# Performance work log

Hardware: AMD Instinct MI355X
Metric: run time of the kernel (lower is better)

## Reference

```python
import jax, jax.numpy as jnp
import numpy as np

NH = 16          # num_attention_heads
NOPE = 128       # qk_nope_head_dim
ROPE = 64        # qk_rope_head_dim
QHD = NOPE + ROPE  # q_head_dim = 192
VD = 128         # v_head_dim
QLR = 1536       # q_lora_rank
KVLR = 512       # kv_lora_rank
HID = 2048
B, S = 1, 2048
THETA = 10000.0
EPS = 1e-6


def rms_norm(x, w, eps=EPS):
    xf = x.astype(jnp.float32)
    var = jnp.mean(xf * xf, axis=-1, keepdims=True)
    return (w * (xf * jax.lax.rsqrt(var + eps)).astype(x.dtype))


def _deinterleave(x):
    # view(..., d//2, 2).transpose(-1, -2).reshape(..., d): evens then odds
    return jnp.concatenate([x[..., 0::2], x[..., 1::2]], axis=-1)


def _rotate_half(x):
    h = x.shape[-1] // 2
    return jnp.concatenate([-x[..., h:], x[..., :h]], axis=-1)


def setup_inputs() -> dict:
    key = jax.random.key(0)
    ks = jax.random.split(key, 6)
    s = 0.02
    return {
        'hidden_states': jax.random.normal(ks[0], (B, S, HID), jnp.float32),
        'position_ids': jnp.arange(S, dtype=jnp.int32)[None, :],
        'Wqa': jax.random.normal(ks[1], (HID, QLR), jnp.float32) * s,
        'qa_ln_w': jnp.ones((QLR,), jnp.float32),
        'Wqb': jax.random.normal(ks[2], (QLR, NH * QHD), jnp.float32) * s,
        'Wkva': jax.random.normal(ks[3], (HID, KVLR + ROPE), jnp.float32) * s,
        'kv_ln_w': jnp.ones((KVLR,), jnp.float32),
        'Wkvb': jax.random.normal(ks[4], (KVLR, NH * (NOPE + VD)), jnp.float32) * s,
        'Wo': jax.random.normal(ks[5], (NH * VD, HID), jnp.float32) * s,
    }


def reference(hidden_states, position_ids, Wqa, qa_ln_w, Wqb, Wkva, kv_ln_w, Wkvb, Wo):
    b, s, _ = hidden_states.shape
    # Q path: low-rank down -> RMSNorm -> up
    q = rms_norm(hidden_states @ Wqa, qa_ln_w) @ Wqb
    q = q.reshape(b, s, NH, QHD).transpose(0, 2, 1, 3)          # (b,h,s,192)
    q_nope, q_pe = q[..., :NOPE], q[..., NOPE:]
    # KV path: compressed kv + shared rope key
    ckv = hidden_states @ Wkva                                   # (b,s,576)
    c_kv, k_pe = ckv[..., :KVLR], ckv[..., KVLR:]
    k_pe = k_pe.reshape(b, s, 1, ROPE).transpose(0, 2, 1, 3)     # (b,1,s,64)
    kv = rms_norm(c_kv, kv_ln_w) @ Wkvb
    kv = kv.reshape(b, s, NH, NOPE + VD).transpose(0, 2, 1, 3)   # (b,h,s,256)
    k_nope, v = kv[..., :NOPE], kv[..., NOPE:]
    # partial RoPE on the 64-dim rope slices
    inv_freq = 1.0 / (THETA ** (jnp.arange(0, ROPE, 2, dtype=jnp.float32) / ROPE))
    t = jnp.arange(s, dtype=jnp.float32)
    emb = jnp.concatenate([jnp.outer(t, inv_freq)] * 2, axis=-1)  # (s,64)
    cos = jnp.cos(emb)[position_ids][:, None]                     # (b,1,s,64)
    sin = jnp.sin(emb)[position_ids][:, None]
    q_pe = _deinterleave(q_pe)
    k_pe = _deinterleave(k_pe)
    q_pe = q_pe * cos + _rotate_half(q_pe) * sin
    k_pe = k_pe * cos + _rotate_half(k_pe) * sin
    query = jnp.concatenate([q_nope, q_pe], axis=-1)                       # (b,h,s,192)
    key = jnp.concatenate([k_nope, jnp.broadcast_to(k_pe, (b, NH, s, ROPE))], axis=-1)
    # causal attention, softmax_scale = q_head_dim**-0.5
    scale = QHD ** (-0.5)
    scores = jnp.einsum('bhqd,bhkd->bhqk', query, key) * scale
    mask = jnp.tril(jnp.ones((s, s), dtype=bool))
    scores = jnp.where(mask, scores, jnp.finfo(scores.dtype).min)
    probs = jax.nn.softmax(scores, axis=-1)
    attn = jnp.einsum('bhqk,bhkd->bhqd', probs, v)               # (b,h,s,128)
    out = attn.transpose(0, 2, 1, 3).reshape(b, s, NH * VD) @ Wo  # (b,s,hid)
    return out
```

## Files before the change

### kernel.cpp

```cpp
#include <hip/hip_runtime.h>
#include <hip/hip_bf16.h>

typedef unsigned short u16;
typedef _Float16 h16;
typedef h16 h16x8 __attribute__((ext_vector_type(8)));
typedef h16 h16x4 __attribute__((ext_vector_type(4)));
typedef float f32x4 __attribute__((ext_vector_type(4)));

#define S_LEN 2048
#define QLR   1536
#define KVLR  512
#define NHEAD 16
#define QHD   192
#define QHS   200
#define VDIM  128
#define SCALE 0.07216878364870322f
#define FREQC (-0.4152410118609203f)

__device__ __forceinline__ void gld16(const h16* g, h16* l){
  __builtin_amdgcn_global_load_lds((__attribute__((address_space(1))) const void*)g,
                                   (__attribute__((address_space(3))) void*)l, 16, 0, 0);
}

__global__ __launch_bounds__(256) void k_cvt(const float* __restrict__ in, h16* __restrict__ out, int n4){
  int i = blockIdx.x * 256 + threadIdx.x;
  if (i < n4){
    float4 v = ((const float4*)in)[i];
    h16x4 o = { (h16)v.x, (h16)v.y, (h16)v.z, (h16)v.w };
    ((h16x4*)out)[i] = o;
  }
}

__global__ __launch_bounds__(256) void k_tc(const float* __restrict__ W, h16* __restrict__ WT, int K, int N){
  __shared__ float t[64][65];
  int k0 = blockIdx.y * 64, n0 = blockIdx.x * 64;
  int tid = threadIdx.x;
  int r = tid >> 4, c4 = (tid & 15) * 4;
#pragma unroll
  for (int it = 0; it < 4; it++){
    float4 v = *(const float4*)(W + (size_t)(k0 + it*16 + r) * N + n0 + c4);
    t[it*16+r][c4] = v.x; t[it*16+r][c4+1] = v.y; t[it*16+r][c4+2] = v.z; t[it*16+r][c4+3] = v.w;
  }
  __syncthreads();
  int n = tid >> 2, k16 = (tid & 3) * 16;
  h16x8 o0, o1;
#pragma unroll
  for (int e = 0; e < 8; e++){ o0[e] = (h16)t[k16 + e][n]; o1[e] = (h16)t[k16 + 8 + e][n]; }
  h16* dst = WT + (size_t)(n0 + n) * K + k0 + k16;
  *(h16x8*)dst = o0;
  *(h16x8*)(dst + 8) = o1;
}

__device__ __forceinline__ void gemm_core(const h16* __restrict__ A, const h16* __restrict__ B,
    int K, int m0, int n0, h16* As, h16* Bs, f32x4 (&acc)[4][4]){
  const int tid = threadIdx.x;
  const int lane = tid & 63, quad = lane >> 4, lr = lane & 15;
  const int wid = tid >> 6;
  const int wr = (wid >> 1) * 64, wc = (wid & 1) * 64;
  const int sr = tid >> 2, scc = (tid & 3) * 8;
  const h16* Ag = A + (size_t)(m0 + sr) * K + scc;
  const h16* Bg = B + (size_t)(n0 + sr) * K + scc;
  for (int kt = 0; kt < K; kt += 32){
    gld16(Ag + kt,                 &As[tid * 8]);
    gld16(Ag + (size_t)64*K + kt,  &As[2048 + tid * 8]);
    gld16(Bg + kt,                 &Bs[tid * 8]);
    gld16(Bg + (size_t)64*K + kt,  &Bs[2048 + tid * 8]);
    __syncthreads();
    h16x8 af[4], bfr[4];
#pragma unroll
    for (int r = 0; r < 4; r++) af[r]  = *(const h16x8*)&As[(wr + r*16 + lr) * 32 + quad * 8];
#pragma unroll
    for (int c = 0; c < 4; c++) bfr[c] = *(const h16x8*)&Bs[(wc + c*16 + lr) * 32 + quad * 8];
#pragma unroll
    for (int r = 0; r < 4; r++)
#pragma unroll
      for (int c = 0; c < 4; c++)
        acc[r][c] = __builtin_amdgcn_mfma_f32_16x16x32_f16(af[r], bfr[c], acc[r][c], 0, 0, 0);
    __syncthreads();
  }
}

template<bool OF32>
__global__ __launch_bounds__(256) void k_gemm(const h16* __restrict__ A, const h16* __restrict__ B,
                                              void* __restrict__ Cv, int N, int K){
  __shared__ __attribute__((aligned(16))) h16 As[128*32];
  __shared__ __attribute__((aligned(16))) h16 Bs[128*32];
  const int m0 = blockIdx.y * 128, n0 = blockIdx.x * 128;
  f32x4 acc[4][4] = {};
  gemm_core(A, B, K, m0, n0, As, Bs, acc);
  const int lane = threadIdx.x & 63, quad = lane >> 4, lr = lane & 15;
  const int wid = threadIdx.x >> 6;
  const int wr = (wid >> 1) * 64, wc = (wid & 1) * 64;
#pragma unroll
  for (int r = 0; r < 4; r++)
#pragma unroll
    for (int c = 0; c < 4; c++){
      int row = m0 + wr + r*16 + quad*4;
      int col = n0 + wc + c*16 + lr;
#pragma unroll
      for (int i = 0; i < 4; i++){
        float val = acc[r][c][i];
        if (OF32) ((float*)Cv)[(size_t)(row + i) * N + col] = val;
        else      ((h16*)Cv)[(size_t)(row + i) * N + col] = (h16)val;
      }
    }
}

__global__ __launch_bounds__(256) void k_gemm_q(const h16* __restrict__ A, const h16* __restrict__ B,
      h16* __restrict__ Qh, const float* __restrict__ cst, const float* __restrict__ snt){
  __shared__ __attribute__((aligned(16))) h16 As[128*32];
  __shared__ __attribute__((aligned(16))) h16 Bs[128*32];
  const int m0 = blockIdx.y * 128, n0 = blockIdx.x * 128;
  f32x4 acc[4][4] = {};
  gemm_core(A, B, QLR, m0, n0, As, Bs, acc);
  const int lane = threadIdx.x & 63, quad = lane >> 4, lr = lane & 15;
  const int wid = threadIdx.x >> 6;
  const int wr = (wid >> 1) * 64, wc = (wid & 1) * 64;
#pragma unroll
  for (int r = 0; r < 4; r++)
#pragma unroll
    for (int c = 0; c < 4; c++){
      int row0 = m0 + wr + r*16 + quad*4;
      int cg = n0 + wc + c*16 + lr;
      int head = cg / 192;
      int inner = cg - head*192;
      h16* outb = Qh + ((size_t)head*S_LEN)*QHS;
      if (inner < 128){
#pragma unroll
        for (int i = 0; i < 4; i++)
          outb[(size_t)(row0+i)*QHS + inner] = (h16)(acc[r][c][i] * SCALE);
      } else {
        int d = (inner - 128) >> 1;
        int isY = inner & 1;
        int ocol = (isY ? 160 : 128) + d;
#pragma unroll
        for (int i = 0; i < 4; i++){
          int rr = row0 + i;
          float cs = cst[rr*32 + d], sn = snt[rr*32 + d];
          float v = acc[r][c][i];
          float w = __shfl_xor(v, 1);
          float out = isY ? (v*cs + w*sn) : (v*cs - w*sn);
          outb[(size_t)rr*QHS + ocol] = (h16)(out * SCALE);
        }
      }
    }
}

__global__ __launch_bounds__(256) void k_gemm_kv(const h16* __restrict__ A, const h16* __restrict__ B,
      h16* __restrict__ Kh, h16* __restrict__ VT){
  __shared__ __attribute__((aligned(16))) h16 As[128*32];
  __shared__ __attribute__((aligned(16))) h16 Bs[128*32];
  __shared__ __attribute__((aligned(16))) h16 tsm[128*132];
  const int m0 = blockIdx.y * 128, n0 = blockIdx.x * 128;
  f32x4 acc[4][4] = {};
  gemm_core(A, B, KVLR, m0, n0, As, Bs, acc);
  const int tid = threadIdx.x;
  const int lane = tid & 63, quad = lane >> 4, lr = lane & 15;
  const int wid = tid >> 6;
  const int wr = (wid >> 1) * 64, wc = (wid & 1) * 64;
  const int head = n0 >> 8;
  if ((n0 & 128) == 0){
#pragma unroll
    for (int r = 0; r < 4; r++)
#pragma unroll
      for (int c = 0; c < 4; c++){
        int row0 = m0 + wr + r*16 + quad*4;
        int inner = wc + c*16 + lr;
#pragma unroll
        for (int i = 0; i < 4; i++)
          Kh[((size_t)head*S_LEN + row0 + i)*QHS + inner] = (h16)acc[r][c][i];
      }
  } else {
#pragma unroll
    for (int r = 0; r < 4; r++)
#pragma unroll
      for (int c = 0; c < 4; c++){
        int lrow = wr + r*16 + quad*4;
        int dv = wc + c*16 + lr;
#pragma unroll
        for (int i = 0; i < 4; i++)
          tsm[(lrow + i)*132 + dv] = (h16)acc[r][c][i];
      }
    __syncthreads();
    int dv = tid >> 1, sh = (tid & 1) * 64;
    h16* vout = VT + ((size_t)(head*VDIM + dv))*S_LEN + m0 + sh;
#pragma unroll
    for (int ko = 0; ko < 8; ko++){
      h16x8 o;
#pragma unroll
      for (int e = 0; e < 8; e++) o[e] = tsm[(sh + ko*8 + e)*132 + dv];
      *(h16x8*)(vout + ((ko*8 + 8*(dv & 7)) & 63)) = o;
    }
  }
}

__global__ __launch_bounds__(256) void k_norm(const h16* __restrict__ Cc,
      const float* __restrict__ qw, const float* __restrict__ kw, const int* __restrict__ pos_ids,
      h16* __restrict__ qln, h16* __restrict__ kvln, h16* __restrict__ Kh,
      float* __restrict__ cst, float* __restrict__ snt){
  const int s = blockIdx.x, tid = threadIdx.x;
  __shared__ float red[8];
  __shared__ h16 kpe_s[64];
  const h16* c1 = Cc + (size_t)s * 2176;
  float v[6]; float ss = 0.f;
#pragma unroll
  for (int i = 0; i < 6; i++){ v[i] = (float)c1[tid + i*256]; ss += v[i]*v[i]; }
  for (int off = 32; off > 0; off >>= 1) ss += __shfl_down(ss, off);
  if ((tid & 63) == 0) red[tid >> 6] = ss;
  __syncthreads();
  float rq = rsqrtf((red[0]+red[1]+red[2]+red[3]) / (float)QLR + 1e-6f);
#pragma unroll
  for (int i = 0; i < 6; i++)
    qln[(size_t)s * QLR + tid + i*256] = (h16)(qw[tid + i*256] * v[i] * rq);

  const h16* ck = c1 + QLR;
  float w0 = (float)ck[tid], w1 = (float)ck[tid + 256];
  float ss2 = w0*w0 + w1*w1;
  for (int off = 32; off > 0; off >>= 1) ss2 += __shfl_down(ss2, off);
  if ((tid & 63) == 0) red[4 + (tid >> 6)] = ss2;
  __syncthreads();
  float rk = rsqrtf((red[4]+red[5]+red[6]+red[7]) / (float)KVLR + 1e-6f);
  kvln[(size_t)s * KVLR + tid]       = (h16)(kw[tid] * w0 * rk);
  kvln[(size_t)s * KVLR + tid + 256] = (h16)(kw[tid + 256] * w1 * rk);

  if (tid < 32){
    int d = tid;
    float x = (float)ck[KVLR + 2*d];
    float y = (float)ck[KVLR + 2*d + 1];
    float a = (float)pos_ids[s] * exp2f(FREQC * (float)d);
    float cs = cosf(a), sn = sinf(a);
    cst[s*32 + d] = cs; snt[s*32 + d] = sn;
    kpe_s[d]      = (h16)(x*cs - y*sn);
    kpe_s[32 + d] = (h16)(y*cs + x*sn);
  }
  __syncthreads();
  {
    int h = tid >> 4, seg = (tid & 15) * 4;
    h16x4 o = { kpe_s[seg], kpe_s[seg+1], kpe_s[seg+2], kpe_s[seg+3] };
    *(h16x4*)&Kh[((size_t)h*S_LEN + s)*QHS + 128 + seg] = o;
  }
}

__global__ __launch_bounds__(256, 2) void k_flash(const h16* __restrict__ Qh, const h16* __restrict__ Kh,
      const h16* __restrict__ VT, h16* __restrict__ Opart, float* __restrict__ ml){
  const int tile = 15 - blockIdx.x;
  const int h = blockIdx.y;
  const int p = blockIdx.z;
  const int jcount = 2*tile + 2;
  const int jlo = p * 8;
  if (jlo >= jcount) return;
  const int jhi = min(jlo + 8, jcount);
  const int m0 = tile * 128;
  __shared__ __attribute__((aligned(16))) h16 Ksm[64*QHS];
  __shared__ __attribute__((aligned(16))) h16 Vsm[144*64];
  __shared__ __attribute__((aligned(16))) h16 Psm[128*72];
  const int tid = threadIdx.x, wid = tid >> 6, lane = tid & 63, quad = lane >> 4, lr = lane & 15;

  {
    h16x4 one4 = { (h16)1.f, (h16)1.f, (h16)1.f, (h16)1.f };
    *(h16x4*)&Vsm[128*64 + tid*4] = one4;
  }

  const h16* Qbase = Qh + ((size_t)h*S_LEN + m0)*QHS;
  h16x8 qf[2][6];
#pragma unroll
  for (int rt = 0; rt < 2; rt++)
#pragma unroll
    for (int ks = 0; ks < 6; ks++)
      qf[rt][ks] = *(const h16x8*)(Qbase + (size_t)(wid*32 + rt*16 + lr)*QHS + ks*32 + quad*8);

  float mst[2][4];
  f32x4 oacc[2][9] = {};
#pragma unroll
  for (int rt = 0; rt < 2; rt++)
#pragma unroll
    for (int i = 0; i < 4; i++) mst[rt][i] = -1e30f;

  for (int j = jlo; j < jhi; ++j){
    const h16* Kg = Kh + ((size_t)h*S_LEN + j*64)*QHS;
#pragma unroll
    for (int i = 0; i < 6; i++) gld16(Kg + i*2048 + tid*8, &Ksm[i*2048 + tid*8]);
    if (tid < 64) gld16(Kg + 12288 + tid*8, &Ksm[12288 + tid*8]);
    const h16* Vg = VT + (size_t)h * VDIM * S_LEN + (size_t)j * 64;
#pragma unroll
    for (int i = 0; i < 4; i++)
      gld16(Vg + (size_t)(i*32 + (tid >> 3)) * S_LEN + (tid & 7)*8, &Vsm[i*2048 + tid*8]);
    __syncthreads();

    f32x4 sc[2][4] = {};
#pragma unroll
    for (int ks = 0; ks < 6; ks++)
#pragma unroll
      for (int ct = 0; ct < 4; ct++){
        h16x8 kf = *(const h16x8*)&Ksm[(ct*16 + lr)*QHS + ks*32 + quad*8];
        sc[0][ct] = __builtin_amdgcn_mfma_f32_16x16x32_f16(qf[0][ks], kf, sc[0][ct], 0,0,0);
        sc[1][ct] = __builtin_amdgcn_mfma_f32_16x16x32_f16(qf[1][ks], kf, sc[1][ct], 0,0,0);
      }

    if (j >= 2*tile){
#pragma unroll
      for (int rt = 0; rt < 2; rt++)
#pragma unroll
        for (int ct = 0; ct < 4; ct++){
          int kcol = j*64 + ct*16 + lr;
#pragma unroll
          for (int i = 0; i < 4; i++)
            if (kcol > m0 + wid*32 + rt*16 + quad*4 + i) sc[rt][ct][i] = -1e30f;
        }
    }

#pragma unroll
    for (int rt = 0; rt < 2; rt++){
      float al[4];
#pragma unroll
      for (int i = 0; i < 4; i++){
        float m = fmaxf(fmaxf(sc[rt][0][i], sc[rt][1][i]), fmaxf(sc[rt][2][i], sc[rt][3][i]));
#pragma unroll
        for (int off = 1; off < 16; off <<= 1) m = fmaxf(m, __shfl_xor(m, off));
        float mn = fmaxf(fmaxf(mst[rt][i], m), -1e29f);
        al[i] = __expf(mst[rt][i] - mn);
        mst[rt][i] = mn;
      }
#pragma unroll
      for (int ct = 0; ct < 4; ct++)
#pragma unroll
        for (int i = 0; i < 4; i++)
          Psm[(wid*32 + rt*16 + quad*4 + i)*72 + ct*16 + lr] = (h16)__expf(sc[rt][ct][i] - mst[rt][i]);
#pragma unroll
      for (int oc = 0; oc < 9; oc++)
#pragma unroll
        for (int i = 0; i < 4; i++) oacc[rt][oc][i] *= al[i];
    }

#pragma unroll
    for (int ks2 = 0; ks2 < 2; ks2++){
      h16x8 pf0 = *(const h16x8*)&Psm[(wid*32 + lr)*72      + ks2*32 + quad*8];
      h16x8 pf1 = *(const h16x8*)&Psm[(wid*32 + 16 + lr)*72 + ks2*32 + quad*8];
      int cv = (ks2*32 + quad*8 + 8*(lr & 7)) & 63;
#pragma unroll
      for (int oc = 0; oc < 9; oc++){
        h16x8 vf = *(const h16x8*)&Vsm[(oc*16 + lr)*64 + cv];
        oacc[0][oc] = __builtin_amdgcn_mfma_f32_16x16x32_f16(pf0, vf, oacc[0][oc], 0,0,0);
        oacc[1][oc] = __builtin_amdgcn_mfma_f32_16x16x32_f16(pf1, vf, oacc[1][oc], 0,0,0);
      }
    }
    __syncthreads();
  }

  const int part = (tile*NHEAD + h)*4 + p;
  h16* Op = Opart + (size_t)part * 16384;
#pragma unroll
  for (int rt = 0; rt < 2; rt++){
#pragma unroll
    for (int oc = 0; oc < 8; oc++)
#pragma unroll
      for (int i = 0; i < 4; i++)
        Op[(wid*32 + rt*16 + quad*4 + i)*128 + oc*16 + lr] = (h16)oacc[rt][oc][i];
    if (lr == 0){
#pragma unroll
      for (int i = 0; i < 4; i++){
        int r = wid*32 + rt*16 + quad*4 + i;
        ml[(size_t)part*256 + r*2]     = mst[rt][i];
        ml[(size_t)part*256 + r*2 + 1] = oacc[rt][8][i];
      }
    }
  }
}

__global__ __launch_bounds__(256) void k_comb(const h16* __restrict__ Opart, const float* __restrict__ ml,
                                              h16* __restrict__ Ob){
  const int t = blockIdx.x, h = blockIdx.y, tid = threadIdx.x;
  const int P = (2*t + 9) >> 3;
  const int r = tid >> 1, c0 = (tid & 1) * 64;
  const int base = (t*NHEAD + h)*4;
  float w[4]; float M = -1e30f, denom = 0.f;
  for (int p = 0; p < P; p++) M = fmaxf(M, ml[(size_t)(base+p)*256 + r*2]);
  for (int p = 0; p < P; p++){
    w[p] = __expf(ml[(size_t)(base+p)*256 + r*2] - M);
    denom += w[p] * ml[(size_t)(base+p)*256 + r*2 + 1];
  }
  float inv = 1.f / denom;
#pragma unroll
  for (int ch = 0; ch < 8; ch++){
    float a[8] = {};
    for (int p = 0; p < P; p++){
      h16x8 v = *(const h16x8*)&Opart[(size_t)(base+p)*16384 + r*128 + c0 + ch*8];
#pragma unroll
      for (int e = 0; e < 8; e++) a[e] += w[p] * (float)v[e];
    }
    h16x8 o;
#pragma unroll
    for (int e = 0; e < 8; e++) o[e] = (h16)(a[e] * inv);
    *(h16x8*)&Ob[((size_t)(t*128 + r))*(NHEAD*VDIM) + h*VDIM + c0 + ch*8] = o;
  }
}

extern "C" void kernel_launch(void* const* d_in, const int* in_sizes, int n_in,
                              void* d_out, int out_size, void* d_ws, size_t ws_size,
                              hipStream_t stream){
  const float* hidden = (const float*)d_in[0];
  const int*   pos    = (const int*)  d_in[1];
  const float* Wqa    = (const float*)d_in[2];
  const float* qaw    = (const float*)d_in[3];
  const float* Wqb    = (const float*)d_in[4];
  const float* Wkva   = (const float*)d_in[5];
  const float* kvw    = (const float*)d_in[6];
  const float* Wkvb   = (const float*)d_in[7];
  const float* Wo     = (const float*)d_in[8];

  h16* ws = (h16*)d_ws;
  size_t off = 0;
  auto take = [&](size_t n){ h16* p = ws + off; off += n; return p; };
  h16* hb    = take(2048ull * 2048);
  h16* WoT   = take(2048ull * 2048);
  h16* Wc    = take(2176ull * 2048);
  h16* WqbT  = take(3072ull * 1536);
  h16* WkvbT = take(4096ull * 512);
  h16* Ccomb = take(2048ull * 2176);
  h16* qln   = take(2048ull * 1536);
  h16* kvln  = take(2048ull * 512);
  float* cst = (float*)take(2048ull * 64);
  float* snt = (float*)take(2048ull * 64);
  h16* Qh    = take(16ull * 2048 * QHS);
  h16* Kh    = take(16ull * 2048 * QHS);
  h16* VT    = take(16ull * 128 * 2048);
  h16* Ob    = hb;
  h16*   Opart = Wc;
  float* mlbuf = (float*)(Wc + 16ull*16*4*16384);

  k_cvt<<<4096, 256, 0, stream>>>(hidden, hb, 1048576);
  k_tc<<<dim3(24, 32), 256, 0, stream>>>(Wqa,  Wc,                 2048, 1536);
  k_tc<<<dim3( 9, 32), 256, 0, stream>>>(Wkva, Wc + 1536ull*2048,  2048, 576);
  k_tc<<<dim3(48, 24), 256, 0, stream>>>(Wqb,  WqbT,  1536, 3072);
  k_tc<<<dim3(64,  8), 256, 0, stream>>>(Wkvb, WkvbT, 512,  4096);
  k_tc<<<dim3(32, 32), 256, 0, stream>>>(Wo,   WoT,   2048, 2048);

  k_gemm<false><<<dim3(17, 16), 256, 0, stream>>>(hb, Wc, Ccomb, 2176, 2048);
  k_norm<<<2048, 256, 0, stream>>>(Ccomb, qaw, kvw, pos, qln, kvln, Kh, cst, snt);
  k_gemm_q <<<dim3(24, 16), 256, 0, stream>>>(qln,  WqbT,  Qh, cst, snt);
  k_gemm_kv<<<dim3(32, 16), 256, 0, stream>>>(kvln, WkvbT, Kh, VT);
  k_flash<<<dim3(16, 16, 4), 256, 0, stream>>>(Qh, Kh, VT, Opart, mlbuf);
  k_comb<<<dim3(16, 16), 256, 0, stream>>>(Opart, mlbuf, Ob);
  k_gemm<true><<<dim3(16, 16), 256, 0, stream>>>(Ob, WoT, d_out, 2048, 2048);
}
```

Before: 383.6 us.

## Keep softmax probabilities in registers via transposed MFMA and lane shuffles

The flash kernel now computes transposed score tiles (K as the A operand), so each lane holds one query row's scores. This makes the row max and row sum reductions shorter and lets the P tile be built with cross-lane shuffles instead of a round trip through shared memory. The ones-column trick for the row sum and the Psm buffer are removed, which lowers LDS use and one column of MFMA work, and the launch bound asks for 3 blocks per CU. The costs are extra shuffle instructions and register pressure that may rise under the tighter occupancy target.

```diff
diff --git a/kernel.cpp b/kernel.cpp
--- a/kernel.cpp
+++ b/kernel.cpp
@@ -241,7 +241,7 @@
   }
 }
 
-__global__ __launch_bounds__(256, 2) void k_flash(const h16* __restrict__ Qh, const h16* __restrict__ Kh,
+__global__ __launch_bounds__(256, 3) void k_flash(const h16* __restrict__ Qh, const h16* __restrict__ Kh,
       const h16* __restrict__ VT, h16* __restrict__ Opart, float* __restrict__ ml){
   const int tile = 15 - blockIdx.x;
   const int h = blockIdx.y;
@@ -252,14 +252,8 @@
   const int jhi = min(jlo + 8, jcount);
   const int m0 = tile * 128;
   __shared__ __attribute__((aligned(16))) h16 Ksm[64*QHS];
-  __shared__ __attribute__((aligned(16))) h16 Vsm[144*64];
-  __shared__ __attribute__((aligned(16))) h16 Psm[128*72];
+  __shared__ __attribute__((aligned(16))) h16 Vsm[128*64];
   const int tid = threadIdx.x, wid = tid >> 6, lane = tid & 63, quad = lane >> 4, lr = lane & 15;
-
-  {
-    h16x4 one4 = { (h16)1.f, (h16)1.f, (h16)1.f, (h16)1.f };
-    *(h16x4*)&Vsm[128*64 + tid*4] = one4;
-  }
 
   const h16* Qbase = Qh + ((size_t)h*S_LEN + m0)*QHS;
   h16x8 qf[2][6];
@@ -269,12 +263,12 @@
     for (int ks = 0; ks < 6; ks++)
       qf[rt][ks] = *(const h16x8*)(Qbase + (size_t)(wid*32 + rt*16 + lr)*QHS + ks*32 + quad*8);
 
-  float mst[2][4];
-  f32x4 oacc[2][9] = {};
-#pragma unroll
-  for (int rt = 0; rt < 2; rt++)
-#pragma unroll
-    for (int i = 0; i < 4; i++) mst[rt][i] = -1e30f;
+  float mst[2] = {-1e30f, -1e30f}, lst[2] = {0.f, 0.f};
+  f32x4 oacc[2][8] = {};
+
+  const int srcA = (((2*quad)    & 3) << 4) + lr;
+  const int srcB = (((2*quad + 1)& 3) << 4) + lr;
+  const bool loq = (quad < 2);
 
   for (int j = jlo; j < jhi; ++j){
     const h16* Kg = Kh + ((size_t)h*S_LEN + j*64)*QHS;
@@ -293,55 +287,78 @@
 #pragma unroll
       for (int ct = 0; ct < 4; ct++){
         h16x8 kf = *(const h16x8*)&Ksm[(ct*16 + lr)*QHS + ks*32 + quad*8];
-        sc[0][ct] = __builtin_amdgcn_mfma_f32_16x16x32_f16(qf[0][ks], kf, sc[0][ct], 0,0,0);
-        sc[1][ct] = __builtin_amdgcn_mfma_f32_16x16x32_f16(qf[1][ks], kf, sc[1][ct], 0,0,0);
+        sc[0][ct] = __builtin_amdgcn_mfma_f32_16x16x32_f16(kf, qf[0][ks], sc[0][ct], 0,0,0);
+        sc[1][ct] = __builtin_amdgcn_mfma_f32_16x16x32_f16(kf, qf[1][ks], sc[1][ct], 0,0,0);
       }
 
     if (j >= 2*tile){
 #pragma unroll
-      for (int rt = 0; rt < 2; rt++)
+      for (int rt = 0; rt < 2; rt++){
+        int qabs = m0 + wid*32 + rt*16 + lr;
 #pragma unroll
         for (int ct = 0; ct < 4; ct++){
-          int kcol = j*64 + ct*16 + lr;
+          int kv0 = j*64 + ct*16 + quad*4;
 #pragma unroll
           for (int i = 0; i < 4; i++)
-            if (kcol > m0 + wid*32 + rt*16 + quad*4 + i) sc[rt][ct][i] = -1e30f;
+            if (kv0 + i > qabs) sc[rt][ct][i] = -1e30f;
         }
-    }
-
+      }
+    }
+
+    long long pk[2][4];
 #pragma unroll
     for (int rt = 0; rt < 2; rt++){
-      float al[4];
-#pragma unroll
-      for (int i = 0; i < 4; i++){
-        float m = fmaxf(fmaxf(sc[rt][0][i], sc[rt][1][i]), fmaxf(sc[rt][2][i], sc[rt][3][i]));
-#pragma unroll
-        for (int off = 1; off < 16; off <<= 1) m = fmaxf(m, __shfl_xor(m, off));
-        float mn = fmaxf(fmaxf(mst[rt][i], m), -1e29f);
-        al[i] = __expf(mst[rt][i] - mn);
-        mst[rt][i] = mn;
-      }
+      float m = -1e30f;
 #pragma unroll
       for (int ct = 0; ct < 4; ct++)
 #pragma unroll
-        for (int i = 0; i < 4; i++)
-          Psm[(wid*32 + rt*16 + quad*4 + i)*72 + ct*16 + lr] = (h16)__expf(sc[rt][ct][i] - mst[rt][i]);
-#pragma unroll
-      for (int oc = 0; oc < 9; oc++)
-#pragma unroll
-        for (int i = 0; i < 4; i++) oacc[rt][oc][i] *= al[i];
+        for (int i = 0; i < 4; i++) m = fmaxf(m, sc[rt][ct][i]);
+      m = fmaxf(m, __shfl_xor(m, 16));
+      m = fmaxf(m, __shfl_xor(m, 32));
+      float mn = fmaxf(fmaxf(mst[rt], m), -1e29f);
+      float al = __expf(mst[rt] - mn);
+      mst[rt] = mn;
+      float rs = 0.f;
+#pragma unroll
+      for (int ct = 0; ct < 4; ct++){
+        h16x4 e4;
+#pragma unroll
+        for (int i = 0; i < 4; i++){
+          float e = __expf(sc[rt][ct][i] - mn);
+          rs += e;
+          e4[i] = (h16)e;
+        }
+        __builtin_memcpy(&pk[rt][ct], &e4, 8);
+      }
+      rs += __shfl_xor(rs, 16);
+      rs += __shfl_xor(rs, 32);
+      lst[rt] = lst[rt]*al + rs;
+#pragma unroll
+      for (int oc = 0; oc < 8; oc++)
+#pragma unroll
+        for (int i = 0; i < 4; i++) oacc[rt][oc][i] *= al;
     }
 
 #pragma unroll
     for (int ks2 = 0; ks2 < 2; ks2++){
-      h16x8 pf0 = *(const h16x8*)&Psm[(wid*32 + lr)*72      + ks2*32 + quad*8];
-      h16x8 pf1 = *(const h16x8*)&Psm[(wid*32 + 16 + lr)*72 + ks2*32 + quad*8];
+      h16x8 pfr[2];
+#pragma unroll
+      for (int rt = 0; rt < 2; rt++){
+        long long la = __shfl(pk[rt][2*ks2],     srcA);
+        long long lb = __shfl(pk[rt][2*ks2 + 1], srcA);
+        long long ha = __shfl(pk[rt][2*ks2],     srcB);
+        long long hb = __shfl(pk[rt][2*ks2 + 1], srcB);
+        long long lo = loq ? la : lb;
+        long long hi = loq ? ha : hb;
+        __builtin_memcpy(&pfr[rt],               &lo, 8);
+        __builtin_memcpy(((char*)&pfr[rt]) + 8,  &hi, 8);
+      }
       int cv = (ks2*32 + quad*8 + 8*(lr & 7)) & 63;
 #pragma unroll
-      for (int oc = 0; oc < 9; oc++){
+      for (int oc = 0; oc < 8; oc++){
         h16x8 vf = *(const h16x8*)&Vsm[(oc*16 + lr)*64 + cv];
-        oacc[0][oc] = __builtin_amdgcn_mfma_f32_16x16x32_f16(pf0, vf, oacc[0][oc], 0,0,0);
-        oacc[1][oc] = __builtin_amdgcn_mfma_f32_16x16x32_f16(pf1, vf, oacc[1][oc], 0,0,0);
+        oacc[0][oc] = __builtin_amdgcn_mfma_f32_16x16x32_f16(vf, pfr[0], oacc[0][oc], 0,0,0);
+        oacc[1][oc] = __builtin_amdgcn_mfma_f32_16x16x32_f16(vf, pfr[1], oacc[1][oc], 0,0,0);
       }
     }
     __syncthreads();
@@ -351,18 +368,15 @@
   h16* Op = Opart + (size_t)part * 16384;
 #pragma unroll
   for (int rt = 0; rt < 2; rt++){
-#pragma unroll
-    for (int oc = 0; oc < 8; oc++)
-#pragma unroll
-      for (int i = 0; i < 4; i++)
-        Op[(wid*32 + rt*16 + quad*4 + i)*128 + oc*16 + lr] = (h16)oacc[rt][oc][i];
-    if (lr == 0){
-#pragma unroll
-      for (int i = 0; i < 4; i++){
-        int r = wid*32 + rt*16 + quad*4 + i;
-        ml[(size_t)part*256 + r*2]     = mst[rt][i];
-        ml[(size_t)part*256 + r*2 + 1] = oacc[rt][8][i];
-      }
+    int r = wid*32 + rt*16 + lr;
+#pragma unroll
+    for (int oc = 0; oc < 8; oc++){
+      h16x4 o = { (h16)oacc[rt][oc][0], (h16)oacc[rt][oc][1], (h16)oacc[rt][oc][2], (h16)oacc[rt][oc][3] };
+      *(h16x4*)&Op[r*128 + oc*16 + quad*4] = o;
+    }
+    if (quad == 0){
+      ml[(size_t)part*256 + r*2]     = mst[rt];
+      ml[(size_t)part*256 + r*2 + 1] = lst[rt];
     }
   }
 }
```

Measured after the change: 408.6 us. 1.07x slower.
